# Kernel optimization log

Hardware: AMD Instinct MI355X
Metric: run time of the kernel (lower is better)

Reference implementation:

```python
import jax, jax.numpy as jnp
import numpy as np

LN_EPS = 1e-5

def _layer_norm(x, w, b):
    m = jnp.mean(x, axis=-1, keepdims=True)
    v = jnp.mean(jnp.square(x - m), axis=-1, keepdims=True)
    return (x - m) * jax.lax.rsqrt(v + LN_EPS) * w + b

def setup_inputs() -> dict:
    key = jax.random.key(0)
    ks = jax.random.split(key, 6)
    B, T, D, H = 64, 512, 512, 512
    x = jax.random.normal(ks[0], (B, T, D), dtype=jnp.float32)
    h = jax.random.normal(ks[1], (B, H), dtype=jnp.float32)
    # orthogonal-ish init approximated by scaled normal (math-equivalent shapes)
    w_ih = jax.random.normal(ks[2], (3 * H, D), dtype=jnp.float32) / np.sqrt(D)
    b_ih = jnp.zeros((3 * H,), dtype=jnp.float32)
    w_hh = jax.random.normal(ks[3], (3 * H, H), dtype=jnp.float32) / np.sqrt(H)
    b_hh = jnp.zeros((3 * H,), dtype=jnp.float32)
    ln_r_w = jnp.ones((H,), jnp.float32); ln_r_b = jnp.zeros((H,), jnp.float32)
    ln_z_w = jnp.ones((H,), jnp.float32); ln_z_b = jnp.zeros((H,), jnp.float32)
    ln_n_w = jnp.ones((H,), jnp.float32); ln_n_b = jnp.zeros((H,), jnp.float32)
    return dict(x=x, h=h, w_ih=w_ih, b_ih=b_ih, w_hh=w_hh, b_hh=b_hh,
                ln_r_w=ln_r_w, ln_r_b=ln_r_b, ln_z_w=ln_z_w, ln_z_b=ln_z_b,
                ln_n_w=ln_n_w, ln_n_b=ln_n_b)

def reference(x, h, w_ih, b_ih, w_hh, b_hh, ln_r_w, ln_r_b, ln_z_w, ln_z_b, ln_n_w, ln_n_b):
    H = h.shape[-1]
    # precompute input gate projections for all timesteps: [B, T, 3H] -> [T, B, 3H]
    x_gates_all = jnp.einsum('btd,gd->btg', x, w_ih) + b_ih
    x_gates_all = jnp.swapaxes(x_gates_all, 0, 1)

    def step(h, x_gates):
        h_gates = jnp.matmul(h, w_hh.T) + b_hh
        x_r, x_z, x_n = jnp.split(x_gates, 3, axis=-1)
        h_r, h_z, h_n = jnp.split(h_gates, 3, axis=-1)
        r = jax.nn.sigmoid(_layer_norm(x_r + h_r, ln_r_w, ln_r_b))
        z = jax.nn.sigmoid(_layer_norm(x_z + h_z, ln_z_w, ln_z_b))
        n = jnp.tanh(_layer_norm(x_n + r * h_n, ln_n_w, ln_n_b))
        h_new = (1.0 - z) * n + z * h
        return h_new, h_new

    h_last, out_tbh = jax.lax.scan(step, h, x_gates_all)
    out = jnp.swapaxes(out_tbh, 0, 1)  # [B, T, H]
    return out, h_last
```

## Files before the change

### kernel.cpp

```cpp
#include <hip/hip_runtime.h>
#include <hip/hip_bf16.h>

#define B_ 64
#define T_ 512
#define D_ 512
#define H_ 512
#define G3 1536
#define NBLK 16

typedef float f32x4 __attribute__((ext_vector_type(4)));
typedef __bf16 bf16x8 __attribute__((ext_vector_type(8)));

#define LDSP 56
#define WPITCH 520

union bfpack { bf16x8 v; __hip_bfloat16 h[8]; };

__device__ inline bf16x8 cvt8(const float* __restrict__ p) {
    float4 f0 = *(const float4*)p;
    float4 f1 = *(const float4*)(p + 4);
    bfpack u;
    u.h[0] = __float2bfloat16(f0.x); u.h[1] = __float2bfloat16(f0.y);
    u.h[2] = __float2bfloat16(f0.z); u.h[3] = __float2bfloat16(f0.w);
    u.h[4] = __float2bfloat16(f1.x); u.h[5] = __float2bfloat16(f1.y);
    u.h[6] = __float2bfloat16(f1.z); u.h[7] = __float2bfloat16(f1.w);
    return u.v;
}

__global__ void k0_init(const float* __restrict__ h_in,
                        __hip_bfloat16* __restrict__ hb,
                        unsigned int* __restrict__ ctr) {
    int i = blockIdx.x * blockDim.x + threadIdx.x;
    if (i < B_ * H_) hb[i] = __float2bfloat16(h_in[i]);
    if (i < 1024)    ctr[i] = 0u;
}

__global__ __launch_bounds__(256) void k1_xgemm(
    const float* __restrict__ X, const float* __restrict__ W,
    const float* __restrict__ bias, __hip_bfloat16* __restrict__ XG)
{
    __shared__ __align__(16) __hip_bfloat16 la[128 * LDSP];
    __shared__ __align__(16) __hip_bfloat16 lb[128 * LDSP];
    int tid = threadIdx.x, bx = blockIdx.x;
    int m0 = (bx / 12) * 128, n0 = (bx % 12) * 128;
    int wave = tid >> 6, lane = tid & 63;
    int wh = wave >> 1, ww = wave & 1;
    int l15 = lane & 15, kq = lane >> 4;

    f32x4 acc[4][4];
    #pragma unroll
    for (int i = 0; i < 4; i++)
        #pragma unroll
        for (int j = 0; j < 4; j++) acc[i][j] = (f32x4){0.f, 0.f, 0.f, 0.f};

    for (int kt = 0; kt < 16; ++kt) {
        int k0 = kt * 32;
        for (int s = tid; s < 512; s += 256) {
            int r = s >> 2, c = s & 3;
            *(bf16x8*)&la[r * LDSP + c * 8] = cvt8(&X[(size_t)(m0 + r) * D_ + k0 + c * 8]);
            *(bf16x8*)&lb[r * LDSP + c * 8] = cvt8(&W[(size_t)(n0 + r) * D_ + k0 + c * 8]);
        }
        __syncthreads();
        bf16x8 af[4], bq[4];
        #pragma unroll
        for (int i = 0; i < 4; i++)
            af[i] = *(const bf16x8*)&la[(wh * 64 + i * 16 + l15) * LDSP + kq * 8];
        #pragma unroll
        for (int j = 0; j < 4; j++)
            bq[j] = *(const bf16x8*)&lb[(ww * 64 + j * 16 + l15) * LDSP + kq * 8];
        #pragma unroll
        for (int i = 0; i < 4; i++)
            #pragma unroll
            for (int j = 0; j < 4; j++)
                acc[i][j] = __builtin_amdgcn_mfma_f32_16x16x32_bf16(af[i], bq[j], acc[i][j], 0, 0, 0);
        __syncthreads();
    }
    #pragma unroll
    for (int i = 0; i < 4; i++)
        #pragma unroll
        for (int j = 0; j < 4; j++)
            #pragma unroll
            for (int r = 0; r < 4; r++) {
                int m = m0 + wh * 64 + i * 16 + kq * 4 + r;
                int n = n0 + ww * 64 + j * 16 + l15;
                int b = m >> 9, t = m & 511;
                XG[((size_t)t * B_ + b) * G3 + n] = __float2bfloat16(acc[i][j][r] + bias[n]);
            }
}

__global__ __launch_bounds__(512, 1) void k2_recur(
    const float* __restrict__ h_in, const float* __restrict__ Whh,
    const float* __restrict__ b_hh,
    const float* __restrict__ lnrw, const float* __restrict__ lnrb,
    const float* __restrict__ lnzw, const float* __restrict__ lnzb,
    const float* __restrict__ lnnw, const float* __restrict__ lnnb,
    const __hip_bfloat16* __restrict__ XG,
    float* __restrict__ HG, __hip_bfloat16* __restrict__ HB,
    unsigned int* __restrict__ ctr, float* __restrict__ out)
{
    __shared__ __align__(16) __hip_bfloat16 lw[96 * WPITCH];

    const int tid = threadIdx.x;
    const int blk = blockIdx.x;
    const int n0 = blk * 96;
    const int s0 = blk * 4;

    for (int idx = tid; idx < 96 * 64; idx += 512) {
        int row = idx >> 6, ch = idx & 63;
        *(bf16x8*)&lw[row * WPITCH + ch * 8] = cvt8(&Whh[(size_t)(n0 + row) * H_ + ch * 8]);
    }

    const int w = tid >> 6, lane = tid & 63;
    const int l15 = lane & 15, kq = lane >> 4;
    const int mt = w >> 1;
    const int nj0 = (w & 1) * 3;

    const int b = s0 + w;
    const int c0 = lane * 8;

    float bhr[8], bhz[8], bhn[8], wr[8], br_[8], wz[8], bz_[8], wn[8], bn_[8], hf[8];
    if (w < 4) {
        #pragma unroll
        for (int q = 0; q < 2; q++) {
            float4 t0 = *(const float4*)&b_hh[c0 + 4 * q];
            float4 t1 = *(const float4*)&b_hh[512 + c0 + 4 * q];
            float4 t2 = *(const float4*)&b_hh[1024 + c0 + 4 * q];
            float4 t3 = *(const float4*)&lnrw[c0 + 4 * q];
            float4 t4 = *(const float4*)&lnrb[c0 + 4 * q];
            float4 t5 = *(const float4*)&lnzw[c0 + 4 * q];
            float4 t6 = *(const float4*)&lnzb[c0 + 4 * q];
            float4 t7 = *(const float4*)&lnnw[c0 + 4 * q];
            float4 t8 = *(const float4*)&lnnb[c0 + 4 * q];
            float4 t9 = *(const float4*)&h_in[b * H_ + c0 + 4 * q];
            bhr[4*q]=t0.x; bhr[4*q+1]=t0.y; bhr[4*q+2]=t0.z; bhr[4*q+3]=t0.w;
            bhz[4*q]=t1.x; bhz[4*q+1]=t1.y; bhz[4*q+2]=t1.z; bhz[4*q+3]=t1.w;
            bhn[4*q]=t2.x; bhn[4*q+1]=t2.y; bhn[4*q+2]=t2.z; bhn[4*q+3]=t2.w;
            wr [4*q]=t3.x; wr [4*q+1]=t3.y; wr [4*q+2]=t3.z; wr [4*q+3]=t3.w;
            br_[4*q]=t4.x; br_[4*q+1]=t4.y; br_[4*q+2]=t4.z; br_[4*q+3]=t4.w;
            wz [4*q]=t5.x; wz [4*q+1]=t5.y; wz [4*q+2]=t5.z; wz [4*q+3]=t5.w;
            bz_[4*q]=t6.x; bz_[4*q+1]=t6.y; bz_[4*q+2]=t6.z; bz_[4*q+3]=t6.w;
            wn [4*q]=t7.x; wn [4*q+1]=t7.y; wn [4*q+2]=t7.z; wn [4*q+3]=t7.w;
            bn_[4*q]=t8.x; bn_[4*q+1]=t8.y; bn_[4*q+2]=t8.z; bn_[4*q+3]=t8.w;
            hf [4*q]=t9.x; hf [4*q+1]=t9.y; hf [4*q+2]=t9.z; hf [4*q+3]=t9.w;
        }
    }
    __syncthreads();

    const float inv = 1.0f / 512.0f;

    for (int t = 0; t < T_; ++t) {
        bf16x8 afr[16];
        {
            const __hip_bfloat16* hrow = HB + (mt * 16 + l15) * H_ + kq * 8;
            #pragma unroll
            for (int kt = 0; kt < 16; kt++) afr[kt] = *(const bf16x8*)(hrow + kt * 32);
        }
        f32x4 a0 = {0,0,0,0}, a1 = {0,0,0,0}, a2 = {0,0,0,0};
        #pragma unroll
        for (int kt = 0; kt < 16; kt++) {
            bf16x8 b0 = *(const bf16x8*)&lw[((nj0    ) * 16 + l15) * WPITCH + kt * 32 + kq * 8];
            bf16x8 b1 = *(const bf16x8*)&lw[((nj0 + 1) * 16 + l15) * WPITCH + kt * 32 + kq * 8];
            bf16x8 b2 = *(const bf16x8*)&lw[((nj0 + 2) * 16 + l15) * WPITCH + kt * 32 + kq * 8];
            a0 = __builtin_amdgcn_mfma_f32_16x16x32_bf16(afr[kt], b0, a0, 0, 0, 0);
            a1 = __builtin_amdgcn_mfma_f32_16x16x32_bf16(afr[kt], b1, a1, 0, 0, 0);
            a2 = __builtin_amdgcn_mfma_f32_16x16x32_bf16(afr[kt], b2, a2, 0, 0, 0);
        }
        {
            int rowb = mt * 16 + kq * 4;
            int colb = n0 + nj0 * 16 + l15;
            #pragma unroll
            for (int r = 0; r < 4; r++) {
                HG[(rowb + r) * G3 + colb     ] = a0[r];
                HG[(rowb + r) * G3 + colb + 16] = a1[r];
                HG[(rowb + r) * G3 + colb + 32] = a2[r];
            }
        }
        __syncthreads();
        if (tid == 0)
            __hip_atomic_fetch_add(&ctr[2 * t], 1u, __ATOMIC_RELEASE, __HIP_MEMORY_SCOPE_AGENT);
        bf16x8 xr8 = {}, xz8 = {}, xn8 = {};
        if (w < 4) {
            const __hip_bfloat16* xgrow = XG + ((size_t)t * B_ + b) * G3;
            xr8 = *(const bf16x8*)&xgrow[c0];
            xz8 = *(const bf16x8*)&xgrow[512 + c0];
            xn8 = *(const bf16x8*)&xgrow[1024 + c0];
        }
        if (tid == 0)
            while (__hip_atomic_load(&ctr[2 * t], __ATOMIC_RELAXED, __HIP_MEMORY_SCOPE_AGENT) < NBLK) {}
        __builtin_amdgcn_fence(__ATOMIC_ACQUIRE, "agent");
        __syncthreads();

        float hnew[8];
        if (w < 4) {
            const float* hgb = HG + (size_t)b * G3;
            float hr[8], hz[8], hn[8];
            #pragma unroll
            for (int q = 0; q < 2; q++) {
                float4 r4 = *(const float4*)&hgb[c0 + 4 * q];
                float4 z4 = *(const float4*)&hgb[512 + c0 + 4 * q];
                float4 n4 = *(const float4*)&hgb[1024 + c0 + 4 * q];
                hr[4*q]=r4.x; hr[4*q+1]=r4.y; hr[4*q+2]=r4.z; hr[4*q+3]=r4.w;
                hz[4*q]=z4.x; hz[4*q+1]=z4.y; hz[4*q+2]=z4.z; hz[4*q+3]=z4.w;
                hn[4*q]=n4.x; hn[4*q+1]=n4.y; hn[4*q+2]=n4.z; hn[4*q+3]=n4.w;
            }
            bfpack xr, xz, xn; xr.v = xr8; xz.v = xz8; xn.v = xn8;
            float ar[8], az[8], anv[8];
            float sr = 0.f, ssr = 0.f, sz = 0.f, ssz = 0.f;
            #pragma unroll
            for (int j = 0; j < 8; j++) {
                ar[j] = __bfloat162float(xr.h[j]) + hr[j] + bhr[j];
                az[j] = __bfloat162float(xz.h[j]) + hz[j] + bhz[j];
                sr += ar[j]; ssr += ar[j] * ar[j];
                sz += az[j]; ssz += az[j] * az[j];
            }
            #pragma unroll
            for (int off = 32; off; off >>= 1) {
                sr += __shfl_xor(sr, off); ssr += __shfl_xor(ssr, off);
                sz += __shfl_xor(sz, off); ssz += __shfl_xor(ssz, off);
            }
            float mr = sr * inv, vr = ssr * inv - mr * mr, rstd_r = rsqrtf(vr + 1e-5f);
            float mz = sz * inv, vz = ssz * inv - mz * mz, rstd_z = rsqrtf(vz + 1e-5f);
            float rg[8], zg[8];
            float sn = 0.f, ssn = 0.f;
            #pragma unroll
            for (int j = 0; j < 8; j++) {
                rg[j] = 1.f / (1.f + __expf(-((ar[j] - mr) * rstd_r * wr[j] + br_[j])));
                zg[j] = 1.f / (1.f + __expf(-((az[j] - mz) * rstd_z * wz[j] + bz_[j])));
                anv[j] = __bfloat162float(xn.h[j]) + rg[j] * (hn[j] + bhn[j]);
                sn += anv[j]; ssn += anv[j] * anv[j];
            }
            #pragma unroll
            for (int off = 32; off; off >>= 1) {
                sn += __shfl_xor(sn, off); ssn += __shfl_xor(ssn, off);
            }
            float mn = sn * inv, vn = ssn * inv - mn * mn, rstd_n = rsqrtf(vn + 1e-5f);
            bfpack hb8;
            #pragma unroll
            for (int j = 0; j < 8; j++) {
                float ng = tanhf((anv[j] - mn) * rstd_n * wn[j] + bn_[j]);
                hnew[j] = (1.f - zg[j]) * ng + zg[j] * hf[j];
                hf[j] = hnew[j];
                hb8.h[j] = __float2bfloat16(hnew[j]);
            }
            *(bf16x8*)&HB[b * H_ + c0] = hb8.v;
        }
        __syncthreads();
        if (tid == 0)
            __hip_atomic_fetch_add(&ctr[2 * t + 1], 1u, __ATOMIC_RELEASE, __HIP_MEMORY_SCOPE_AGENT);
        if (w < 4) {
            float* op = out + ((size_t)b * T_ + t) * H_ + c0;
            *(float4*)op       = make_float4(hnew[0], hnew[1], hnew[2], hnew[3]);
            *(float4*)(op + 4) = make_float4(hnew[4], hnew[5], hnew[6], hnew[7]);
            if (t == T_ - 1) {
                float* fp = out + (size_t)B_ * T_ * H_ + b * H_ + c0;
                *(float4*)fp       = make_float4(hnew[0], hnew[1], hnew[2], hnew[3]);
                *(float4*)(fp + 4) = make_float4(hnew[4], hnew[5], hnew[6], hnew[7]);
            }
        }
        if (tid == 0)
            while (__hip_atomic_load(&ctr[2 * t + 1], __ATOMIC_RELAXED, __HIP_MEMORY_SCOPE_AGENT) < NBLK) {}
        __builtin_amdgcn_fence(__ATOMIC_ACQUIRE, "agent");
        __syncthreads();
    }
}

extern "C" void kernel_launch(void* const* d_in, const int* in_sizes, int n_in,
                              void* d_out, int out_size, void* d_ws, size_t ws_size,
                              hipStream_t stream)
{
    const float* x    = (const float*)d_in[0];
    const float* h    = (const float*)d_in[1];
    const float* w_ih = (const float*)d_in[2];
    const float* b_ih = (const float*)d_in[3];
    const float* w_hh = (const float*)d_in[4];
    const float* b_hh = (const float*)d_in[5];
    const float* lnrw = (const float*)d_in[6];
    const float* lnrb = (const float*)d_in[7];
    const float* lnzw = (const float*)d_in[8];
    const float* lnzb = (const float*)d_in[9];
    const float* lnnw = (const float*)d_in[10];
    const float* lnnb = (const float*)d_in[11];
    float* out = (float*)d_out;

    char* ws = (char*)d_ws;
    __hip_bfloat16* XG = (__hip_bfloat16*)ws;
    float*          HG = (float*)(ws + 100663296);
    __hip_bfloat16* HB = (__hip_bfloat16*)(ws + 101056512);
    unsigned int*  CTR = (unsigned int*)(ws + 101122048);

    k0_init<<<128, 256, 0, stream>>>(h, HB, CTR);
    k1_xgemm<<<3072, 256, 0, stream>>>(x, w_ih, b_ih, XG);
    k2_recur<<<NBLK, 512, 0, stream>>>(h, w_hh, b_hh,
        lnrw, lnrb, lnzw, lnzb, lnnw, lnnb, XG, HG, HB, CTR, out);
}
```

Baseline: 5.790 ms.

## Pipeline GRU recurrence over batch groups with per-block flag handshakes

The single all-block counter barrier pair per timestep becomes per-group flag arrays. The batch is split into 4 groups of 16 rows and each block handles one row per group. Each group's GEMM slice waits only on that group's previous elementwise results, and its elementwise phase waits only on that group's GEMM flags. This is meant to overlap the GEMM and LayerNorm phases across groups and replace counter atomics with one wave polling 16 flags. In exchange, each block now does 8 barrier waits per step instead of 2. Only 6 waves run MFMA and 1 wave does the elementwise work, so per-block parallelism drops.

```diff
diff --git a/kernel.cpp b/kernel.cpp
--- a/kernel.cpp
+++ b/kernel.cpp
@@ -7,6 +7,8 @@
 #define H_ 512
 #define G3 1536
 #define NBLK 16
+#define NG 4
+#define SPG 16
 
 typedef float f32x4 __attribute__((ext_vector_type(4)));
 typedef __bf16 bf16x8 __attribute__((ext_vector_type(8)));
@@ -29,10 +31,10 @@
 
 __global__ void k0_init(const float* __restrict__ h_in,
                         __hip_bfloat16* __restrict__ hb,
-                        unsigned int* __restrict__ ctr) {
+                        unsigned int* __restrict__ flags) {
     int i = blockIdx.x * blockDim.x + threadIdx.x;
     if (i < B_ * H_) hb[i] = __float2bfloat16(h_in[i]);
-    if (i < 1024)    ctr[i] = 0u;
+    if (i < 128) flags[i] = 0u;
 }
 
 __global__ __launch_bounds__(256) void k1_xgemm(
@@ -96,14 +98,14 @@
     const float* __restrict__ lnnw, const float* __restrict__ lnnb,
     const __hip_bfloat16* __restrict__ XG,
     float* __restrict__ HG, __hip_bfloat16* __restrict__ HB,
-    unsigned int* __restrict__ ctr, float* __restrict__ out)
+    unsigned int* __restrict__ flagsA, unsigned int* __restrict__ flagsB,
+    float* __restrict__ out)
 {
     __shared__ __align__(16) __hip_bfloat16 lw[96 * WPITCH];
 
     const int tid = threadIdx.x;
     const int blk = blockIdx.x;
     const int n0 = blk * 96;
-    const int s0 = blk * 4;
 
     for (int idx = tid; idx < 96 * 64; idx += 512) {
         int row = idx >> 6, ch = idx & 63;
@@ -112,14 +114,11 @@
 
     const int w = tid >> 6, lane = tid & 63;
     const int l15 = lane & 15, kq = lane >> 4;
-    const int mt = w >> 1;
-    const int nj0 = (w & 1) * 3;
-
-    const int b = s0 + w;
+
     const int c0 = lane * 8;
-
-    float bhr[8], bhz[8], bhn[8], wr[8], br_[8], wz[8], bz_[8], wn[8], bn_[8], hf[8];
-    if (w < 4) {
+    float bhr[8], bhz[8], bhn[8], wr[8], br_[8], wz[8], bz_[8], wn[8], bn_[8];
+    float hf[NG][8];
+    if (w == 0) {
         #pragma unroll
         for (int q = 0; q < 2; q++) {
             float4 t0 = *(const float4*)&b_hh[c0 + 4 * q];
@@ -131,7 +130,6 @@
             float4 t6 = *(const float4*)&lnzb[c0 + 4 * q];
             float4 t7 = *(const float4*)&lnnw[c0 + 4 * q];
             float4 t8 = *(const float4*)&lnnb[c0 + 4 * q];
-            float4 t9 = *(const float4*)&h_in[b * H_ + c0 + 4 * q];
             bhr[4*q]=t0.x; bhr[4*q+1]=t0.y; bhr[4*q+2]=t0.z; bhr[4*q+3]=t0.w;
             bhz[4*q]=t1.x; bhz[4*q+1]=t1.y; bhz[4*q+2]=t1.z; bhz[4*q+3]=t1.w;
             bhn[4*q]=t2.x; bhn[4*q+1]=t2.y; bhn[4*q+2]=t2.z; bhn[4*q+3]=t2.w;
@@ -141,7 +139,14 @@
             bz_[4*q]=t6.x; bz_[4*q+1]=t6.y; bz_[4*q+2]=t6.z; bz_[4*q+3]=t6.w;
             wn [4*q]=t7.x; wn [4*q+1]=t7.y; wn [4*q+2]=t7.z; wn [4*q+3]=t7.w;
             bn_[4*q]=t8.x; bn_[4*q+1]=t8.y; bn_[4*q+2]=t8.z; bn_[4*q+3]=t8.w;
-            hf [4*q]=t9.x; hf [4*q+1]=t9.y; hf [4*q+2]=t9.z; hf [4*q+3]=t9.w;
+        }
+        #pragma unroll
+        for (int g = 0; g < NG; g++) {
+            int s = g * SPG + blk;
+            float4 h0 = *(const float4*)&h_in[s * H_ + c0];
+            float4 h1 = *(const float4*)&h_in[s * H_ + c0 + 4];
+            hf[g][0]=h0.x; hf[g][1]=h0.y; hf[g][2]=h0.z; hf[g][3]=h0.w;
+            hf[g][4]=h1.x; hf[g][5]=h1.y; hf[g][6]=h1.z; hf[g][7]=h1.w;
         }
     }
     __syncthreads();
@@ -149,118 +154,127 @@
     const float inv = 1.0f / 512.0f;
 
     for (int t = 0; t < T_; ++t) {
-        bf16x8 afr[16];
-        {
-            const __hip_bfloat16* hrow = HB + (mt * 16 + l15) * H_ + kq * 8;
-            #pragma unroll
-            for (int kt = 0; kt < 16; kt++) afr[kt] = *(const bf16x8*)(hrow + kt * 32);
-        }
-        f32x4 a0 = {0,0,0,0}, a1 = {0,0,0,0}, a2 = {0,0,0,0};
-        #pragma unroll
-        for (int kt = 0; kt < 16; kt++) {
-            bf16x8 b0 = *(const bf16x8*)&lw[((nj0    ) * 16 + l15) * WPITCH + kt * 32 + kq * 8];
-            bf16x8 b1 = *(const bf16x8*)&lw[((nj0 + 1) * 16 + l15) * WPITCH + kt * 32 + kq * 8];
-            bf16x8 b2 = *(const bf16x8*)&lw[((nj0 + 2) * 16 + l15) * WPITCH + kt * 32 + kq * 8];
-            a0 = __builtin_amdgcn_mfma_f32_16x16x32_bf16(afr[kt], b0, a0, 0, 0, 0);
-            a1 = __builtin_amdgcn_mfma_f32_16x16x32_bf16(afr[kt], b1, a1, 0, 0, 0);
-            a2 = __builtin_amdgcn_mfma_f32_16x16x32_bf16(afr[kt], b2, a2, 0, 0, 0);
-        }
-        {
-            int rowb = mt * 16 + kq * 4;
-            int colb = n0 + nj0 * 16 + l15;
-            #pragma unroll
-            for (int r = 0; r < 4; r++) {
-                HG[(rowb + r) * G3 + colb     ] = a0[r];
-                HG[(rowb + r) * G3 + colb + 16] = a1[r];
-                HG[(rowb + r) * G3 + colb + 32] = a2[r];
-            }
-        }
-        __syncthreads();
-        if (tid == 0)
-            __hip_atomic_fetch_add(&ctr[2 * t], 1u, __ATOMIC_RELEASE, __HIP_MEMORY_SCOPE_AGENT);
-        bf16x8 xr8 = {}, xz8 = {}, xn8 = {};
-        if (w < 4) {
-            const __hip_bfloat16* xgrow = XG + ((size_t)t * B_ + b) * G3;
-            xr8 = *(const bf16x8*)&xgrow[c0];
-            xz8 = *(const bf16x8*)&xgrow[512 + c0];
-            xn8 = *(const bf16x8*)&xgrow[1024 + c0];
-        }
-        if (tid == 0)
-            while (__hip_atomic_load(&ctr[2 * t], __ATOMIC_RELAXED, __HIP_MEMORY_SCOPE_AGENT) < NBLK) {}
-        __builtin_amdgcn_fence(__ATOMIC_ACQUIRE, "agent");
-        __syncthreads();
-
-        float hnew[8];
-        if (w < 4) {
-            const float* hgb = HG + (size_t)b * G3;
-            float hr[8], hz[8], hn[8];
-            #pragma unroll
-            for (int q = 0; q < 2; q++) {
-                float4 r4 = *(const float4*)&hgb[c0 + 4 * q];
-                float4 z4 = *(const float4*)&hgb[512 + c0 + 4 * q];
-                float4 n4 = *(const float4*)&hgb[1024 + c0 + 4 * q];
-                hr[4*q]=r4.x; hr[4*q+1]=r4.y; hr[4*q+2]=r4.z; hr[4*q+3]=r4.w;
-                hz[4*q]=z4.x; hz[4*q+1]=z4.y; hz[4*q+2]=z4.z; hz[4*q+3]=z4.w;
-                hn[4*q]=n4.x; hn[4*q+1]=n4.y; hn[4*q+2]=n4.z; hn[4*q+3]=n4.w;
-            }
-            bfpack xr, xz, xn; xr.v = xr8; xz.v = xz8; xn.v = xn8;
-            float ar[8], az[8], anv[8];
-            float sr = 0.f, ssr = 0.f, sz = 0.f, ssz = 0.f;
-            #pragma unroll
-            for (int j = 0; j < 8; j++) {
-                ar[j] = __bfloat162float(xr.h[j]) + hr[j] + bhr[j];
-                az[j] = __bfloat162float(xz.h[j]) + hz[j] + bhz[j];
-                sr += ar[j]; ssr += ar[j] * ar[j];
-                sz += az[j]; ssz += az[j] * az[j];
-            }
-            #pragma unroll
-            for (int off = 32; off; off >>= 1) {
-                sr += __shfl_xor(sr, off); ssr += __shfl_xor(ssr, off);
-                sz += __shfl_xor(sz, off); ssz += __shfl_xor(ssz, off);
-            }
-            float mr = sr * inv, vr = ssr * inv - mr * mr, rstd_r = rsqrtf(vr + 1e-5f);
-            float mz = sz * inv, vz = ssz * inv - mz * mz, rstd_z = rsqrtf(vz + 1e-5f);
-            float rg[8], zg[8];
-            float sn = 0.f, ssn = 0.f;
-            #pragma unroll
-            for (int j = 0; j < 8; j++) {
-                rg[j] = 1.f / (1.f + __expf(-((ar[j] - mr) * rstd_r * wr[j] + br_[j])));
-                zg[j] = 1.f / (1.f + __expf(-((az[j] - mz) * rstd_z * wz[j] + bz_[j])));
-                anv[j] = __bfloat162float(xn.h[j]) + rg[j] * (hn[j] + bhn[j]);
-                sn += anv[j]; ssn += anv[j] * anv[j];
-            }
-            #pragma unroll
-            for (int off = 32; off; off >>= 1) {
-                sn += __shfl_xor(sn, off); ssn += __shfl_xor(ssn, off);
-            }
-            float mn = sn * inv, vn = ssn * inv - mn * mn, rstd_n = rsqrtf(vn + 1e-5f);
-            bfpack hb8;
-            #pragma unroll
-            for (int j = 0; j < 8; j++) {
-                float ng = tanhf((anv[j] - mn) * rstd_n * wn[j] + bn_[j]);
-                hnew[j] = (1.f - zg[j]) * ng + zg[j] * hf[j];
-                hf[j] = hnew[j];
-                hb8.h[j] = __float2bfloat16(hnew[j]);
-            }
-            *(bf16x8*)&HB[b * H_ + c0] = hb8.v;
-        }
-        __syncthreads();
-        if (tid == 0)
-            __hip_atomic_fetch_add(&ctr[2 * t + 1], 1u, __ATOMIC_RELEASE, __HIP_MEMORY_SCOPE_AGENT);
-        if (w < 4) {
-            float* op = out + ((size_t)b * T_ + t) * H_ + c0;
-            *(float4*)op       = make_float4(hnew[0], hnew[1], hnew[2], hnew[3]);
-            *(float4*)(op + 4) = make_float4(hnew[4], hnew[5], hnew[6], hnew[7]);
-            if (t == T_ - 1) {
-                float* fp = out + (size_t)B_ * T_ * H_ + b * H_ + c0;
-                *(float4*)fp       = make_float4(hnew[0], hnew[1], hnew[2], hnew[3]);
-                *(float4*)(fp + 4) = make_float4(hnew[4], hnew[5], hnew[6], hnew[7]);
-            }
-        }
-        if (tid == 0)
-            while (__hip_atomic_load(&ctr[2 * t + 1], __ATOMIC_RELAXED, __HIP_MEMORY_SCOPE_AGENT) < NBLK) {}
-        __builtin_amdgcn_fence(__ATOMIC_ACQUIRE, "agent");
-        __syncthreads();
+        for (int g = 0; g < NG; ++g) {
+            if (w == 0) {
+                unsigned want = (unsigned)t;
+                unsigned v;
+                do {
+                    v = (lane < NBLK)
+                        ? __hip_atomic_load(&flagsB[g * NBLK + lane], __ATOMIC_RELAXED, __HIP_MEMORY_SCOPE_AGENT)
+                        : want;
+                } while (!__all(v == want));
+            }
+            __syncthreads();
+            __builtin_amdgcn_fence(__ATOMIC_ACQUIRE, "agent");
+            if (w >= 1 && w <= 6) {
+                int nt = w - 1;
+                bf16x8 afr[16];
+                const __hip_bfloat16* hrow = HB + (g * SPG + l15) * H_ + kq * 8;
+                #pragma unroll
+                for (int kt = 0; kt < 16; kt++) afr[kt] = *(const bf16x8*)(hrow + kt * 32);
+                f32x4 a0 = {0, 0, 0, 0};
+                #pragma unroll
+                for (int kt = 0; kt < 16; kt++) {
+                    bf16x8 b0 = *(const bf16x8*)&lw[(nt * 16 + l15) * WPITCH + kt * 32 + kq * 8];
+                    a0 = __builtin_amdgcn_mfma_f32_16x16x32_bf16(afr[kt], b0, a0, 0, 0, 0);
+                }
+                int rowb = g * SPG + kq * 4;
+                int colb = n0 + nt * 16 + l15;
+                #pragma unroll
+                for (int r = 0; r < 4; r++)
+                    HG[(size_t)(rowb + r) * G3 + colb] = a0[r];
+            }
+            __syncthreads();
+            if (tid == 0)
+                __hip_atomic_store(&flagsA[g * NBLK + blk], (unsigned)(t + 1),
+                                   __ATOMIC_RELEASE, __HIP_MEMORY_SCOPE_AGENT);
+        }
+        for (int g = 0; g < NG; ++g) {
+            if (w == 0) {
+                unsigned want = (unsigned)(t + 1);
+                unsigned v;
+                do {
+                    v = (lane < NBLK)
+                        ? __hip_atomic_load(&flagsA[g * NBLK + lane], __ATOMIC_RELAXED, __HIP_MEMORY_SCOPE_AGENT)
+                        : want;
+                } while (!__all(v == want));
+            }
+            __syncthreads();
+            __builtin_amdgcn_fence(__ATOMIC_ACQUIRE, "agent");
+            float hnew[8];
+            const int s = g * SPG + blk;
+            if (w == 0) {
+                const float* hgb = HG + (size_t)s * G3;
+                const __hip_bfloat16* xgrow = XG + ((size_t)t * B_ + s) * G3;
+                bfpack xr, xz, xn;
+                xr.v = *(const bf16x8*)&xgrow[c0];
+                xz.v = *(const bf16x8*)&xgrow[512 + c0];
+                xn.v = *(const bf16x8*)&xgrow[1024 + c0];
+                float hr[8], hz[8], hn[8];
+                #pragma unroll
+                for (int q = 0; q < 2; q++) {
+                    float4 r4 = *(const float4*)&hgb[c0 + 4 * q];
+                    float4 z4 = *(const float4*)&hgb[512 + c0 + 4 * q];
+                    float4 n4 = *(const float4*)&hgb[1024 + c0 + 4 * q];
+                    hr[4*q]=r4.x; hr[4*q+1]=r4.y; hr[4*q+2]=r4.z; hr[4*q+3]=r4.w;
+                    hz[4*q]=z4.x; hz[4*q+1]=z4.y; hz[4*q+2]=z4.z; hz[4*q+3]=z4.w;
+                    hn[4*q]=n4.x; hn[4*q+1]=n4.y; hn[4*q+2]=n4.z; hn[4*q+3]=n4.w;
+                }
+                float ar[8], az[8], anv[8];
+                float sr = 0.f, ssr = 0.f, sz = 0.f, ssz = 0.f;
+                #pragma unroll
+                for (int j = 0; j < 8; j++) {
+                    ar[j] = __bfloat162float(xr.h[j]) + hr[j] + bhr[j];
+                    az[j] = __bfloat162float(xz.h[j]) + hz[j] + bhz[j];
+                    sr += ar[j]; ssr += ar[j] * ar[j];
+                    sz += az[j]; ssz += az[j] * az[j];
+                }
+                #pragma unroll
+                for (int off = 32; off; off >>= 1) {
+                    sr += __shfl_xor(sr, off); ssr += __shfl_xor(ssr, off);
+                    sz += __shfl_xor(sz, off); ssz += __shfl_xor(ssz, off);
+                }
+                float mr = sr * inv, vr = ssr * inv - mr * mr, rstd_r = rsqrtf(vr + 1e-5f);
+                float mz = sz * inv, vz = ssz * inv - mz * mz, rstd_z = rsqrtf(vz + 1e-5f);
+                float rg[8], zg[8];
+                float sn = 0.f, ssn = 0.f;
+                #pragma unroll
+                for (int j = 0; j < 8; j++) {
+                    rg[j] = 1.f / (1.f + __expf(-((ar[j] - mr) * rstd_r * wr[j] + br_[j])));
+                    zg[j] = 1.f / (1.f + __expf(-((az[j] - mz) * rstd_z * wz[j] + bz_[j])));
+                    anv[j] = __bfloat162float(xn.h[j]) + rg[j] * (hn[j] + bhn[j]);
+                    sn += anv[j]; ssn += anv[j] * anv[j];
+                }
+                #pragma unroll
+                for (int off = 32; off; off >>= 1) {
+                    sn += __shfl_xor(sn, off); ssn += __shfl_xor(ssn, off);
+                }
+                float mn = sn * inv, vn = ssn * inv - mn * mn, rstd_n = rsqrtf(vn + 1e-5f);
+                bfpack hb8;
+                #pragma unroll
+                for (int j = 0; j < 8; j++) {
+                    float ng = tanhf((anv[j] - mn) * rstd_n * wn[j] + bn_[j]);
+                    hnew[j] = (1.f - zg[j]) * ng + zg[j] * hf[g][j];
+                    hf[g][j] = hnew[j];
+                    hb8.h[j] = __float2bfloat16(hnew[j]);
+                }
+                *(bf16x8*)&HB[s * H_ + c0] = hb8.v;
+            }
+            __syncthreads();
+            if (tid == 0)
+                __hip_atomic_store(&flagsB[g * NBLK + blk], (unsigned)(t + 1),
+                                   __ATOMIC_RELEASE, __HIP_MEMORY_SCOPE_AGENT);
+            if (w == 0) {
+                float* op = out + ((size_t)s * T_ + t) * H_ + c0;
+                *(float4*)op       = make_float4(hnew[0], hnew[1], hnew[2], hnew[3]);
+                *(float4*)(op + 4) = make_float4(hnew[4], hnew[5], hnew[6], hnew[7]);
+                if (t == T_ - 1) {
+                    float* fp = out + (size_t)B_ * T_ * H_ + s * H_ + c0;
+                    *(float4*)fp       = make_float4(hnew[0], hnew[1], hnew[2], hnew[3]);
+                    *(float4*)(fp + 4) = make_float4(hnew[4], hnew[5], hnew[6], hnew[7]);
+                }
+            }
+        }
     }
 }
 
@@ -286,10 +300,12 @@
     __hip_bfloat16* XG = (__hip_bfloat16*)ws;
     float*          HG = (float*)(ws + 100663296);
     __hip_bfloat16* HB = (__hip_bfloat16*)(ws + 101056512);
-    unsigned int*  CTR = (unsigned int*)(ws + 101122048);
-
-    k0_init<<<128, 256, 0, stream>>>(h, HB, CTR);
+    unsigned int* FLAGS = (unsigned int*)(ws + 101122048);
+    unsigned int* FLAGSA = FLAGS;
+    unsigned int* FLAGSB = FLAGS + 64;
+
+    k0_init<<<128, 256, 0, stream>>>(h, HB, FLAGS);
     k1_xgemm<<<3072, 256, 0, stream>>>(x, w_ih, b_ih, XG);
     k2_recur<<<NBLK, 512, 0, stream>>>(h, w_hh, b_hh,
-        lnrw, lnrb, lnzw, lnzb, lnnw, lnnb, XG, HG, HB, CTR, out);
-}
+        lnrw, lnrb, lnzw, lnzb, lnnw, lnnb, XG, HG, HB, FLAGSA, FLAGSB, out);
+}
```

New measurement: 18.43 ms. +218.3%, slower.
